# Kernel tuning notes

Hardware: AMD Instinct MI355X
Metric: run time of the kernel (lower is better)

Reference implementation:

```python
import jax, jax.numpy as jnp
import numpy as np

LAMB = 4.0
TH = -4.0 / LAMB  # threshold from APELoss.__init__
LOSS_WEIGHT = 1.0


def setup_inputs() -> dict:
    key = jax.random.key(0)
    k1, k2 = jax.random.split(key)
    N = 151552  # total anchors
    F = 1024    # foreground anchors (placed first so masks have static shape)
    logits = jax.random.normal(k1, (N,), dtype=jnp.float32)
    targets = jnp.concatenate([jnp.ones((F,), jnp.int32), jnp.zeros((N - F,), jnp.int32)])
    ious = jax.random.uniform(k2, (F,), dtype=jnp.float32)
    return {"logits": logits, "targets": targets, "ious": ious, "num_fg": F}


def reference(logits, targets, ious, num_fg):
    # targets is constructed with all fg (==1) in the first num_fg slots,
    # so logits[targets==1] == logits[:num_fg] (static-shape equivalent).
    fg = logits[:num_fg]          # [F] foreground logits
    bg = logits[num_fg:]          # [B] background logits (targets==0)
    p_min = jnp.min(fg)
    rel_bg = bg >= p_min + TH     # relevant background selection

    # Pairwise fg-vs-bg: [F, B]
    diff_bg = (bg[None, :] - fg[:, None]) * LAMB
    neg_mask = rel_bg[None, :] & (bg[None, :] > fg[:, None] + TH)

    # Pairwise fg-vs-fg: [F, F]
    diff_fg = (fg[None, :] - fg[:, None]) * LAMB
    above = fg[None, :] > fg[:, None] + TH
    pos_mask = (ious[None, :] < ious[:, None]) & above   # lower-IoU fg act as negatives
    tp_mask = (ious[None, :] >= ious[:, None]) & above   # higher/equal-IoU fg are TPs

    # rank = sum sigmoid(FP) + sum sigmoid(TP)  (detached in original)
    fp_sum = (jnp.sum(jax.nn.sigmoid(diff_bg) * neg_mask, axis=1)
              + jnp.sum(jax.nn.sigmoid(diff_fg) * pos_mask, axis=1))
    tp_sum = jnp.sum(jax.nn.sigmoid(diff_fg) * tp_mask, axis=1)
    rank = jax.lax.stop_gradient(fp_sum + tp_sum)

    # BCE(sigmoid(z), 0) = -log(1 - sigmoid(z)) = softplus(z)  (stable form)
    dist = (jnp.sum(jax.nn.softplus(diff_bg) * neg_mask, axis=1)
            + jnp.sum(jax.nn.softplus(diff_fg) * pos_mask, axis=1))

    # Original only appends a loss term when FP_dis is non-empty.
    count = jnp.sum(neg_mask, axis=1) + jnp.sum(pos_mask, axis=1)
    valid = count > 0
    safe_rank = jnp.where(valid, rank, 1.0)
    per = jnp.where(valid, dist * ious / safe_rank, 0.0)
    n_valid = jnp.maximum(jnp.sum(valid), 1)

    return LOSS_WEIGHT * jnp.sum(per) / n_valid.astype(per.dtype) / LAMB
```

## Files before the change

### kernel.cpp

```cpp
#include <hip/hip_runtime.h>
#include <hip/hip_bf16.h>


#define APE_LAMB 4.0f
#define APE_KC   5.770780163555856f
#define APE_LN2  0.6931471805599453f
#define NINF     (-__builtin_inff())

__device__ __forceinline__ float exp2g(float x) { return __builtin_amdgcn_exp2f(x); }
__device__ __forceinline__ float log2g(float x) { return __builtin_amdgcn_logf(x); }
__device__ __forceinline__ float rcpg(float x)  { return __builtin_amdgcn_rcpf(x); }

constexpr int   B_BINS  = 2048;
constexpr int   NB      = 16;
constexpr int   TPB     = 256;
constexpr float BIN_LO  = -5.12f;
constexpr float BIN_DL  = 0.005f;
constexpr float BIN_INV = 200.0f;
constexpr float M1SCALE = 268435456.0f;
constexpr float M1INV   = 3.725290298461914e-09f;
constexpr int   ROWS_E  = 4;
constexpr int   ROWS_B  = 4;

__global__ __launch_bounds__(TPB) void ape_build(
    const float* __restrict__ logits, int F, int M,
    int* __restrict__ gCnt, int* __restrict__ gM1, float* __restrict__ bmaxA)
{
    __shared__ int hc[B_BINS];
    __shared__ int hm[B_BINS];
    const int tid = threadIdx.x;
    for (int b = tid; b < B_BINS; b += TPB) { hc[b] = 0; hm[b] = 0; }
    __syncthreads();

    const float* bg = logits + F;
    float bmax = NINF;
    const int stride = gridDim.x * TPB * 4;
    for (int j = ((int)blockIdx.x * TPB + tid) * 4; j < M; j += stride) {
        float v[4];
        if (j + 4 <= M) {
            float4 q = *reinterpret_cast<const float4*>(bg + j);
            v[0] = q.x; v[1] = q.y; v[2] = q.z; v[3] = q.w;
        } else {
#pragma unroll
            for (int k = 0; k < 4; ++k) v[k] = (j + k < M) ? bg[j + k] : NINF;
        }
#pragma unroll
        for (int k = 0; k < 4; ++k) {
            if (j + k >= M) continue;
            float x = v[k];
            bmax = fmaxf(bmax, x);
            int b = (int)((x - BIN_LO) * BIN_INV);
            b = min(max(b, 0), B_BINS - 1);
            float c = fmaf((float)b, BIN_DL, BIN_LO + 0.5f * BIN_DL);
            int q = __float2int_rn((x - c) * M1SCALE);
            atomicAdd(&hc[b], 1);
            atomicAdd(&hm[b], q);
        }
    }
    __syncthreads();
    for (int b = tid; b < B_BINS; b += TPB) {
        int c = hc[b];
        if (c) { atomicAdd(&gCnt[b], c); atomicAdd(&gM1[b], hm[b]); }
    }
    __shared__ float rm[4];
    const int lane = tid & 63, wid = tid >> 6;
    for (int off = 32; off > 0; off >>= 1) bmax = fmaxf(bmax, __shfl_down(bmax, off));
    if (lane == 0) rm[wid] = bmax;
    __syncthreads();
    if (tid == 0)
        bmaxA[blockIdx.x] = fmaxf(fmaxf(rm[0], rm[1]), fmaxf(rm[2], rm[3]));
}

__global__ __launch_bounds__(TPB) void ape_eval(
    const float* __restrict__ logits, const float* __restrict__ ious, int F, int EB,
    const int* __restrict__ gCnt, const int* __restrict__ gM1,
    float* __restrict__ rankB, float* __restrict__ distB,
    float* __restrict__ dist2, float* __restrict__ rank2, float* __restrict__ cnt2)
{
    const int tid  = threadIdx.x;
    const int lane = tid & 63, wid = tid >> 6;

    if ((int)blockIdx.x < EB) {
        __shared__ float2 h[B_BINS];
        for (int b = tid; b < B_BINS; b += TPB)
            h[b] = make_float2((float)gCnt[b], (float)gM1[b] * M1INV);

        const int i0 = (int)blockIdx.x * ROWS_E;
        float fKC[ROWS_E];
#pragma unroll
        for (int r = 0; r < ROWS_E; ++r) {
            int i = i0 + r;
            fKC[r] = (i < F) ? logits[i] * APE_KC : __builtin_inff();
        }
        __syncthreads();

        float rk[ROWS_E], dt[ROWS_E];
#pragma unroll
        for (int r = 0; r < ROWS_E; ++r) { rk[r] = 0.f; dt[r] = 0.f; }

        for (int it = 0; it < B_BINS; it += TPB) {
            const int b = it + tid;
            float2 cm = h[b];
            float cKC  = fmaf((float)b, BIN_DL * APE_KC,
                              (BIN_LO + 0.5f * BIN_DL) * APE_KC);
            float m1x4 = cm.y * APE_LAMB;
            float m1kc = cm.y * APE_KC;
#pragma unroll
            for (int r = 0; r < ROWS_E; ++r) {
                float dl = cKC - fKC[r];
                float dm = (dl > -APE_KC) ? dl : NINF;
                float u  = exp2g(dm);
                float o  = 1.0f + u;
                float rr = rcpg(o);
                float lg = log2g(o);
                float s  = 1.0f - rr;
                rk[r] = fmaf(cm.x, s,  rk[r]);
                rk[r] = fmaf(m1x4, s * rr, rk[r]);
                dt[r] = fmaf(cm.x, lg, dt[r]);
                dt[r] = fmaf(m1kc, s,  dt[r]);
            }
        }

        __shared__ float red[4][ROWS_E * 2];
#pragma unroll
        for (int r = 0; r < ROWS_E; ++r) {
            float a = rk[r], d = dt[r];
            for (int off = 32; off > 0; off >>= 1) {
                a += __shfl_down(a, off);
                d += __shfl_down(d, off);
            }
            if (lane == 0) { red[wid][r*2+0] = a; red[wid][r*2+1] = d; }
        }
        __syncthreads();
        if (tid < ROWS_E * 2) {
            float sum = red[0][tid] + red[1][tid] + red[2][tid] + red[3][tid];
            int r = tid >> 1, q = tid & 1;
            int i = i0 + r;
            if (i < F) {
                if (q == 0) rankB[i] = sum;
                else        distB[i] = sum;
            }
        }
    } else {
        const int i0 = ((int)blockIdx.x - EB) * ROWS_B;
        float fgl[ROWS_B], ioui[ROWS_B];
#pragma unroll
        for (int r = 0; r < ROWS_B; ++r) {
            int i = i0 + r;
            fgl[r]  = (i < F) ? logits[i] * APE_KC : __builtin_inff();
            ioui[r] = (i < F) ? ious[i] : 0.f;
        }
        float dist[ROWS_B], rank[ROWS_B], cnt[ROWS_B];
#pragma unroll
        for (int r = 0; r < ROWS_B; ++r) { dist[r]=0.f; rank[r]=0.f; cnt[r]=0.f; }

        for (int j = tid; j < F; j += TPB) {
            float fjl  = logits[j] * APE_KC;
            float iouj = ious[j];
#pragma unroll
            for (int r = 0; r < ROWS_B; ++r) {
                float dl = fjl - fgl[r];
                bool above = dl > -APE_KC;
                float dm = above ? dl : NINF;
                float u  = exp2g(dm);
                float o  = 1.0f + u;
                float sig = 1.0f - rcpg(o);
                float spl = log2g(o);
                bool pos = iouj < ioui[r];
                rank[r] += sig;
                dist[r] += pos ? spl : 0.f;
                cnt[r]  += (above && pos) ? 1.f : 0.f;
            }
        }
        __shared__ float redf[4][ROWS_B * 3];
#pragma unroll
        for (int r = 0; r < ROWS_B; ++r) {
            float d = dist[r], a = rank[r], c = cnt[r];
            for (int off = 32; off > 0; off >>= 1) {
                d += __shfl_down(d, off);
                a += __shfl_down(a, off);
                c += __shfl_down(c, off);
            }
            if (lane == 0) { redf[wid][r*3+0]=d; redf[wid][r*3+1]=a; redf[wid][r*3+2]=c; }
        }
        __syncthreads();
        if (tid < ROWS_B * 3) {
            float sum = redf[0][tid] + redf[1][tid] + redf[2][tid] + redf[3][tid];
            int r = tid / 3, q = tid % 3;
            int i = i0 + r;
            if (i < F) {
                if      (q == 0) dist2[i] = sum;
                else if (q == 1) rank2[i] = sum;
                else             cnt2[i]  = sum;
            }
        }
    }
}

__global__ __launch_bounds__(TPB) void ape_final(
    const float* __restrict__ logits, const float* __restrict__ ious, int F,
    const float* __restrict__ rankB, const float* __restrict__ distB,
    const float* __restrict__ dist2, const float* __restrict__ rank2,
    const float* __restrict__ cnt2,  const float* __restrict__ bmaxA,
    float* __restrict__ out)
{
    const int tid = threadIdx.x;
    const int lane = tid & 63, wid = tid >> 6;
    __shared__ float gms;
    if (tid == 0) {
        float m = NINF;
        for (int k = 0; k < NB; ++k) m = fmaxf(m, bmaxA[k]);
        gms = m;
    }
    __syncthreads();
    const float gmax = gms;

    float sper = 0.f, sval = 0.f;
    for (int i = tid; i < F; i += TPB) {
        float rkv = rankB[i] + rank2[i];
        float dtv = (distB[i] + dist2[i]) * APE_LN2;
        bool valid = (gmax > logits[i] - 1.0f) || (cnt2[i] > 0.f);
        if (valid) {
            sper += dtv * ious[i] / rkv;
            sval += 1.f;
        }
    }
    __shared__ float rp[4], rv[4];
    for (int off = 32; off > 0; off >>= 1) {
        sper += __shfl_down(sper, off);
        sval += __shfl_down(sval, off);
    }
    if (lane == 0) { rp[wid] = sper; rv[wid] = sval; }
    __syncthreads();
    if (tid == 0) {
        float p = rp[0] + rp[1] + rp[2] + rp[3];
        float v = rv[0] + rv[1] + rv[2] + rv[3];
        out[0] = p / fmaxf(v, 1.f) / APE_LAMB;
    }
}

extern "C" void kernel_launch(void* const* d_in, const int* in_sizes, int n_in,
                              void* d_out, int out_size, void* d_ws, size_t ws_size,
                              hipStream_t stream) {
    const float* logits = (const float*)d_in[0];
    const float* ious   = (const float*)d_in[2];
    const int N = in_sizes[0];
    const int F = in_sizes[2];
    const int M = N - F;

    int*   gCnt  = (int*)d_ws;
    int*   gM1   = gCnt + B_BINS;
    float* bmaxA = (float*)(gM1 + B_BINS);
    float* rankB = bmaxA + NB;
    float* distB = rankB + F;
    float* dist2 = distB + F;
    float* rank2 = dist2 + F;
    float* cnt2  = rank2 + F;

    hipMemsetAsync(gCnt, 0, 2 * B_BINS * sizeof(int), stream);
    ape_build<<<NB, TPB, 0, stream>>>(logits, F, M, gCnt, gM1, bmaxA);

    const int EB = (F + ROWS_E - 1) / ROWS_E;
    const int FB = (F + ROWS_B - 1) / ROWS_B;
    ape_eval<<<EB + FB, TPB, 0, stream>>>(logits, ious, F, EB, gCnt, gM1,
                                          rankB, distB, dist2, rank2, cnt2);
    ape_final<<<1, TPB, 0, stream>>>(logits, ious, F, rankB, distB, dist2, rank2,
                                     cnt2, bmaxA, (float*)d_out);
}
```

Baseline: 24.08 us.

## Restructure into two launches with per-block histograms and last-block final reduction

The memset and the three kernels become two. Phase 1 runs the background histogram blocks alongside the fg-vs-fg pair blocks, and each histogram block writes its own partial histogram as floats, so no global atomics or memset are needed. Phase 2 sums the partial histograms into shared memory, evaluates the bin contributions, then uses an atomic counter so the last block does the final reduction. This removes launch and memset overhead and overlaps the two independent workloads. In exchange every phase-2 block redundantly sums 16 partial histograms, and correctness depends on the fences around the counter.

```diff
diff --git a/kernel.cpp b/kernel.cpp
--- a/kernel.cpp
+++ b/kernel.cpp
@@ -22,127 +22,68 @@
 constexpr int   ROWS_E  = 4;
 constexpr int   ROWS_B  = 4;
 
-__global__ __launch_bounds__(TPB) void ape_build(
-    const float* __restrict__ logits, int F, int M,
-    int* __restrict__ gCnt, int* __restrict__ gM1, float* __restrict__ bmaxA)
-{
-    __shared__ int hc[B_BINS];
-    __shared__ int hm[B_BINS];
-    const int tid = threadIdx.x;
-    for (int b = tid; b < B_BINS; b += TPB) { hc[b] = 0; hm[b] = 0; }
-    __syncthreads();
-
-    const float* bg = logits + F;
-    float bmax = NINF;
-    const int stride = gridDim.x * TPB * 4;
-    for (int j = ((int)blockIdx.x * TPB + tid) * 4; j < M; j += stride) {
-        float v[4];
-        if (j + 4 <= M) {
-            float4 q = *reinterpret_cast<const float4*>(bg + j);
-            v[0] = q.x; v[1] = q.y; v[2] = q.z; v[3] = q.w;
-        } else {
-#pragma unroll
-            for (int k = 0; k < 4; ++k) v[k] = (j + k < M) ? bg[j + k] : NINF;
-        }
-#pragma unroll
-        for (int k = 0; k < 4; ++k) {
-            if (j + k >= M) continue;
-            float x = v[k];
-            bmax = fmaxf(bmax, x);
-            int b = (int)((x - BIN_LO) * BIN_INV);
-            b = min(max(b, 0), B_BINS - 1);
-            float c = fmaf((float)b, BIN_DL, BIN_LO + 0.5f * BIN_DL);
-            int q = __float2int_rn((x - c) * M1SCALE);
-            atomicAdd(&hc[b], 1);
-            atomicAdd(&hm[b], q);
-        }
-    }
-    __syncthreads();
-    for (int b = tid; b < B_BINS; b += TPB) {
-        int c = hc[b];
-        if (c) { atomicAdd(&gCnt[b], c); atomicAdd(&gM1[b], hm[b]); }
-    }
-    __shared__ float rm[4];
-    const int lane = tid & 63, wid = tid >> 6;
-    for (int off = 32; off > 0; off >>= 1) bmax = fmaxf(bmax, __shfl_down(bmax, off));
-    if (lane == 0) rm[wid] = bmax;
-    __syncthreads();
-    if (tid == 0)
-        bmaxA[blockIdx.x] = fmaxf(fmaxf(rm[0], rm[1]), fmaxf(rm[2], rm[3]));
-}
-
-__global__ __launch_bounds__(TPB) void ape_eval(
-    const float* __restrict__ logits, const float* __restrict__ ious, int F, int EB,
-    const int* __restrict__ gCnt, const int* __restrict__ gM1,
-    float* __restrict__ rankB, float* __restrict__ distB,
-    float* __restrict__ dist2, float* __restrict__ rank2, float* __restrict__ cnt2)
+#define ST_AGENT(p, v) __hip_atomic_store((p), (v), __ATOMIC_RELAXED, __HIP_MEMORY_SCOPE_AGENT)
+#define LD_AGENT(p)    __hip_atomic_load((p), __ATOMIC_RELAXED, __HIP_MEMORY_SCOPE_AGENT)
+
+__global__ __launch_bounds__(TPB) void ape_phase1(
+    const float* __restrict__ logits, const float* __restrict__ ious,
+    int F, int M, int chunkH,
+    float* __restrict__ gC, float* __restrict__ gM, float* __restrict__ bmaxA,
+    float* __restrict__ dist2, float* __restrict__ rank2, float* __restrict__ cnt2,
+    int* __restrict__ ctr)
 {
     const int tid  = threadIdx.x;
     const int lane = tid & 63, wid = tid >> 6;
 
-    if ((int)blockIdx.x < EB) {
-        __shared__ float2 h[B_BINS];
-        for (int b = tid; b < B_BINS; b += TPB)
-            h[b] = make_float2((float)gCnt[b], (float)gM1[b] * M1INV);
-
-        const int i0 = (int)blockIdx.x * ROWS_E;
-        float fKC[ROWS_E];
-#pragma unroll
-        for (int r = 0; r < ROWS_E; ++r) {
-            int i = i0 + r;
-            fKC[r] = (i < F) ? logits[i] * APE_KC : __builtin_inff();
-        }
-        __syncthreads();
-
-        float rk[ROWS_E], dt[ROWS_E];
-#pragma unroll
-        for (int r = 0; r < ROWS_E; ++r) { rk[r] = 0.f; dt[r] = 0.f; }
-
-        for (int it = 0; it < B_BINS; it += TPB) {
-            const int b = it + tid;
-            float2 cm = h[b];
-            float cKC  = fmaf((float)b, BIN_DL * APE_KC,
-                              (BIN_LO + 0.5f * BIN_DL) * APE_KC);
-            float m1x4 = cm.y * APE_LAMB;
-            float m1kc = cm.y * APE_KC;
-#pragma unroll
-            for (int r = 0; r < ROWS_E; ++r) {
-                float dl = cKC - fKC[r];
-                float dm = (dl > -APE_KC) ? dl : NINF;
-                float u  = exp2g(dm);
-                float o  = 1.0f + u;
-                float rr = rcpg(o);
-                float lg = log2g(o);
-                float s  = 1.0f - rr;
-                rk[r] = fmaf(cm.x, s,  rk[r]);
-                rk[r] = fmaf(m1x4, s * rr, rk[r]);
-                dt[r] = fmaf(cm.x, lg, dt[r]);
-                dt[r] = fmaf(m1kc, s,  dt[r]);
-            }
-        }
-
-        __shared__ float red[4][ROWS_E * 2];
-#pragma unroll
-        for (int r = 0; r < ROWS_E; ++r) {
-            float a = rk[r], d = dt[r];
-            for (int off = 32; off > 0; off >>= 1) {
-                a += __shfl_down(a, off);
-                d += __shfl_down(d, off);
-            }
-            if (lane == 0) { red[wid][r*2+0] = a; red[wid][r*2+1] = d; }
-        }
-        __syncthreads();
-        if (tid < ROWS_E * 2) {
-            float sum = red[0][tid] + red[1][tid] + red[2][tid] + red[3][tid];
-            int r = tid >> 1, q = tid & 1;
-            int i = i0 + r;
-            if (i < F) {
-                if (q == 0) rankB[i] = sum;
-                else        distB[i] = sum;
-            }
-        }
+    if (blockIdx.x == 0 && tid == 0) *ctr = 0;
+
+    if ((int)blockIdx.x < NB) {
+        __shared__ int hc[B_BINS];
+        __shared__ int hm[B_BINS];
+        for (int b = tid; b < B_BINS; b += TPB) { hc[b] = 0; hm[b] = 0; }
+        __syncthreads();
+
+        const float* bg = logits + F;
+        const int start = (int)blockIdx.x * chunkH;
+        const int end   = min(start + chunkH, M);
+        float bmax = NINF;
+
+        for (int j = start + tid * 4; j < end; j += TPB * 4) {
+            float v[4];
+            if (j + 4 <= end) {
+                float4 q = *reinterpret_cast<const float4*>(bg + j);
+                v[0] = q.x; v[1] = q.y; v[2] = q.z; v[3] = q.w;
+            } else {
+#pragma unroll
+                for (int k = 0; k < 4; ++k) v[k] = (j + k < end) ? bg[j + k] : NINF;
+            }
+#pragma unroll
+            for (int k = 0; k < 4; ++k) {
+                if (j + k >= end) continue;
+                float x = v[k];
+                bmax = fmaxf(bmax, x);
+                int b = (int)((x - BIN_LO) * BIN_INV);
+                b = min(max(b, 0), B_BINS - 1);
+                float c = fmaf((float)b, BIN_DL, BIN_LO + 0.5f * BIN_DL);
+                int q = __float2int_rn((x - c) * M1SCALE);
+                atomicAdd(&hc[b], 1);
+                atomicAdd(&hm[b], q);
+            }
+        }
+        __syncthreads();
+        const int base = (int)blockIdx.x * B_BINS;
+        for (int b = tid; b < B_BINS; b += TPB) {
+            gC[base + b] = (float)hc[b];
+            gM[base + b] = (float)hm[b] * M1INV;
+        }
+        __shared__ float rm[4];
+        for (int off = 32; off > 0; off >>= 1) bmax = fmaxf(bmax, __shfl_down(bmax, off));
+        if (lane == 0) rm[wid] = bmax;
+        __syncthreads();
+        if (tid == 0)
+            bmaxA[blockIdx.x] = fmaxf(fmaxf(rm[0], rm[1]), fmaxf(rm[2], rm[3]));
     } else {
-        const int i0 = ((int)blockIdx.x - EB) * ROWS_B;
+        const int i0 = ((int)blockIdx.x - NB) * ROWS_B;
         float fgl[ROWS_B], ioui[ROWS_B];
 #pragma unroll
         for (int r = 0; r < ROWS_B; ++r) {
@@ -197,15 +138,96 @@
     }
 }
 
-__global__ __launch_bounds__(TPB) void ape_final(
-    const float* __restrict__ logits, const float* __restrict__ ious, int F,
-    const float* __restrict__ rankB, const float* __restrict__ distB,
+__global__ __launch_bounds__(TPB) void ape_phase2(
+    const float* __restrict__ logits, const float* __restrict__ ious, int F, int EB,
+    const float* __restrict__ gC, const float* __restrict__ gM,
+    const float* __restrict__ bmaxA,
     const float* __restrict__ dist2, const float* __restrict__ rank2,
-    const float* __restrict__ cnt2,  const float* __restrict__ bmaxA,
-    float* __restrict__ out)
+    const float* __restrict__ cnt2,
+    float* __restrict__ rankB, float* __restrict__ distB,
+    int* __restrict__ ctr, float* __restrict__ out)
 {
-    const int tid = threadIdx.x;
+    const int tid  = threadIdx.x;
     const int lane = tid & 63, wid = tid >> 6;
+
+    __shared__ float2 h[B_BINS];
+    for (int b = tid; b < B_BINS; b += TPB) {
+        float c = 0.f, m = 0.f;
+#pragma unroll
+        for (int s = 0; s < NB; ++s) {
+            c += gC[s * B_BINS + b];
+            m += gM[s * B_BINS + b];
+        }
+        h[b] = make_float2(c, m);
+    }
+
+    const int i0 = (int)blockIdx.x * ROWS_E;
+    float fKC[ROWS_E];
+#pragma unroll
+    for (int r = 0; r < ROWS_E; ++r) {
+        int i = i0 + r;
+        fKC[r] = (i < F) ? logits[i] * APE_KC : __builtin_inff();
+    }
+    __syncthreads();
+
+    float rk[ROWS_E], dt[ROWS_E];
+#pragma unroll
+    for (int r = 0; r < ROWS_E; ++r) { rk[r] = 0.f; dt[r] = 0.f; }
+
+    for (int it = 0; it < B_BINS; it += TPB) {
+        const int b = it + tid;
+        float2 cm = h[b];
+        float cKC  = fmaf((float)b, BIN_DL * APE_KC, (BIN_LO + 0.5f * BIN_DL) * APE_KC);
+        float m1x4 = cm.y * APE_LAMB;
+        float m1kc = cm.y * APE_KC;
+#pragma unroll
+        for (int r = 0; r < ROWS_E; ++r) {
+            float dl = cKC - fKC[r];
+            float dm = (dl > -APE_KC) ? dl : NINF;
+            float u  = exp2g(dm);
+            float o  = 1.0f + u;
+            float rr = rcpg(o);
+            float lg = log2g(o);
+            float s  = 1.0f - rr;
+            rk[r] = fmaf(cm.x, s,  rk[r]);
+            rk[r] = fmaf(m1x4, s * rr, rk[r]);
+            dt[r] = fmaf(cm.x, lg, dt[r]);
+            dt[r] = fmaf(m1kc, s,  dt[r]);
+        }
+    }
+
+    __shared__ float red[4][ROWS_E * 2];
+#pragma unroll
+    for (int r = 0; r < ROWS_E; ++r) {
+        float a = rk[r], d = dt[r];
+        for (int off = 32; off > 0; off >>= 1) {
+            a += __shfl_down(a, off);
+            d += __shfl_down(d, off);
+        }
+        if (lane == 0) { red[wid][r*2+0] = a; red[wid][r*2+1] = d; }
+    }
+    __syncthreads();
+    if (tid < ROWS_E * 2) {
+        float sum = red[0][tid] + red[1][tid] + red[2][tid] + red[3][tid];
+        int r = tid >> 1, q = tid & 1;
+        int i = i0 + r;
+        if (i < F) {
+            if (q == 0) ST_AGENT(&rankB[i], sum);
+            else        ST_AGENT(&distB[i], sum);
+        }
+    }
+    __syncthreads();
+
+    __shared__ int lastFlag;
+    if (tid == 0) {
+        __threadfence();
+        int old = atomicAdd(ctr, 1);
+        lastFlag = (old == EB - 1) ? 1 : 0;
+    }
+    __syncthreads();
+    if (!lastFlag) return;
+    __threadfence();
+
     __shared__ float gms;
     if (tid == 0) {
         float m = NINF;
@@ -217,8 +239,8 @@
 
     float sper = 0.f, sval = 0.f;
     for (int i = tid; i < F; i += TPB) {
-        float rkv = rankB[i] + rank2[i];
-        float dtv = (distB[i] + dist2[i]) * APE_LN2;
+        float rkv = LD_AGENT(&rankB[i]) + rank2[i];
+        float dtv = (LD_AGENT(&distB[i]) + dist2[i]) * APE_LN2;
         bool valid = (gmax > logits[i] - 1.0f) || (cnt2[i] > 0.f);
         if (valid) {
             sper += dtv * ious[i] / rkv;
@@ -248,22 +270,26 @@
     const int F = in_sizes[2];
     const int M = N - F;
 
-    int*   gCnt  = (int*)d_ws;
-    int*   gM1   = gCnt + B_BINS;
-    float* bmaxA = (float*)(gM1 + B_BINS);
+    float* ws    = (float*)d_ws;
+    float* gC    = ws;
+    float* gM    = gC + NB * B_BINS;
+    float* bmaxA = gM + NB * B_BINS;
     float* rankB = bmaxA + NB;
     float* distB = rankB + F;
     float* dist2 = distB + F;
     float* rank2 = dist2 + F;
     float* cnt2  = rank2 + F;
-
-    hipMemsetAsync(gCnt, 0, 2 * B_BINS * sizeof(int), stream);
-    ape_build<<<NB, TPB, 0, stream>>>(logits, F, M, gCnt, gM1, bmaxA);
-
+    int*   ctr   = (int*)(cnt2 + F);
+
+    int chunkH = ((M + NB - 1) / NB + 3) & ~3;
+    if (chunkH < 4) chunkH = 4;
+
+    const int FB = (F + ROWS_B - 1) / ROWS_B;
     const int EB = (F + ROWS_E - 1) / ROWS_E;
-    const int FB = (F + ROWS_B - 1) / ROWS_B;
-    ape_eval<<<EB + FB, TPB, 0, stream>>>(logits, ious, F, EB, gCnt, gM1,
-                                          rankB, distB, dist2, rank2, cnt2);
-    ape_final<<<1, TPB, 0, stream>>>(logits, ious, F, rankB, distB, dist2, rank2,
-                                     cnt2, bmaxA, (float*)d_out);
+
+    ape_phase1<<<NB + FB, TPB, 0, stream>>>(logits, ious, F, M, chunkH,
+                                            gC, gM, bmaxA, dist2, rank2, cnt2, ctr);
+    ape_phase2<<<EB, TPB, 0, stream>>>(logits, ious, F, EB, gC, gM, bmaxA,
+                                       dist2, rank2, cnt2, rankB, distB, ctr,
+                                       (float*)d_out);
 }
```

Measured after the change: 38.72 us. 60.8% more time.
